# Kernel optimization log

Hardware: AMD Instinct MI355X
Metric: run time of the kernel (lower is better)

Reference implementation:

```python
import jax, jax.numpy as jnp
import numpy as np

B, HH, WW, C = 8, 56, 56, 192
DEPTH = 2
D_IN = 384      # ssm_ratio=2.0 * d_model
R = 12          # dt_rank = ceil(192/16)
HID = 768
L = HH * WW
EPS = 1e-5

PNAMES = ("norm1_w", "norm1_b", "in_proj_w", "conv_w", "conv_b", "x_proj_w",
          "dt_proj_w", "dt_proj_b", "A_log", "Ds", "out_norm_w", "out_norm_b",
          "out_proj_w", "norm2_w", "norm2_b", "fc1_w", "fc1_b", "fc2_w", "fc2_b")


def _mst_bfs_np(fm):
    """Per-image MST (Kruskal) on the 4-connected grid with cosine-distance
    edge weights mapped through exp (MinimumSpanningTree('Cosine', torch.exp)),
    then BFS from node 0. Returns (bfs order, parent-of-ordered-node)."""
    fm = np.asarray(fm, np.float32)
    Bn, H, W, Cc = fm.shape
    Ln = H * W
    idx_out = np.zeros((Bn, Ln), np.int32)
    par_out = np.zeros((Bn, Ln), np.int32)
    ids = np.arange(Ln).reshape(H, W)
    e_u = np.concatenate([ids[:, :-1].ravel(), ids[:-1, :].ravel()])
    e_v = np.concatenate([ids[:, 1:].ravel(), ids[1:, :].ravel()])
    for b in range(Bn):
        f = fm[b].reshape(Ln, Cc)
        nrm = np.linalg.norm(f, axis=1) + 1e-8
        cos = (f[e_u] * f[e_v]).sum(1) / (nrm[e_u] * nrm[e_v])
        wgt = np.exp(1.0 - cos)
        order = np.argsort(wgt, kind="stable")
        uf = np.arange(Ln)
        def find(a):
            while uf[a] != a:
                uf[a] = uf[uf[a]]
                a = uf[a]
            return a
        adj = [[] for _ in range(Ln)]
        cnt = 0
        for e in order:
            u, v = int(e_u[e]), int(e_v[e])
            ru, rv = find(u), find(v)
            if ru != rv:
                uf[ru] = rv
                adj[u].append(v)
                adj[v].append(u)
                cnt += 1
                if cnt == Ln - 1:
                    break
        bfs = np.zeros(Ln, np.int32)
        par = np.zeros(Ln, np.int32)
        visited = np.zeros(Ln, bool)
        visited[0] = True
        head, tail = 0, 1
        while head < tail:
            u = int(bfs[head])
            for v in adj[u]:
                if not visited[v]:
                    visited[v] = True
                    bfs[tail] = v
                    par[tail] = u
                    tail += 1
            head += 1
        idx_out[b] = bfs
        par_out[b] = par
    return idx_out, par_out


def _mst_bfs(x):
    shp = jax.ShapeDtypeStruct((x.shape[0], x.shape[1] * x.shape[2]), jnp.int32)
    return jax.pure_callback(_mst_bfs_np, (shp, shp), jax.lax.stop_gradient(x))


def _ln(x, w, b):
    mu = jnp.mean(x, -1, keepdims=True)
    var = jnp.mean((x - mu) ** 2, -1, keepdims=True)
    return (x - mu) * jax.lax.rsqrt(var + EPS) * w + b


def _tree_scan(feat, w, bfs_idx, bfs_par):
    # feat, w: (B, L, D); bfs_idx/bfs_par: (B, L) int32.
    # Pass 1 (leaf->root): S[p] += w[n] * S[n] in reverse BFS order.
    # Pass 2 (root->leaf): H[n] = S[n] + w[n] * (H[p] - w[n] * S[n]).
    Bn = feat.shape[0]
    bi = jnp.arange(Bn)

    def p1(S, np_):
        n, p = np_
        S = S.at[bi, p].add(w[bi, n] * S[bi, n])
        return S, None

    xs1 = (bfs_idx[:, 1:][:, ::-1].T, bfs_par[:, 1:][:, ::-1].T)
    S, _ = jax.lax.scan(p1, feat, xs1)

    def p2(Hc, np_):
        n, p = np_
        wn, sn = w[bi, n], S[bi, n]
        Hc = Hc.at[bi, n].set(sn + wn * (Hc[bi, p] - wn * sn))
        return Hc, None

    xs2 = (bfs_idx[:, 1:].T, bfs_par[:, 1:].T)
    Hh, _ = jax.lax.scan(p2, S, xs2)
    return Hh


def _layer(x, p, tree):
    bfs_idx, bfs_par = tree
    Bn = x.shape[0]
    # --- Tree_SSM branch (pre-norm) ---
    xn = _ln(x, p["norm1_w"], p["norm1_b"])
    xz = xn @ p["in_proj_w"].T                     # (B,H,W,2*D_IN)
    xs, z = jnp.split(xz, 2, axis=-1)
    xs = jax.lax.conv_general_dilated(
        xs, p["conv_w"], (1, 1), "SAME",
        dimension_numbers=("NHWC", "HWIO", "NHWC"),
        feature_group_count=D_IN) + p["conv_b"]    # depthwise 3x3
    u = jax.nn.silu(xs).reshape(Bn, L, D_IN)       # (B,L,D)
    x_dbl = u @ p["x_proj_w"].T                    # (B,L,R+2), d_state=1
    dts = jax.nn.softplus(x_dbl[..., :R] @ p["dt_proj_w"].T + p["dt_proj_b"])
    Bs, Cs = x_dbl[..., R:R + 1], x_dbl[..., R + 1:R + 2]
    A = -jnp.exp(p["A_log"][:, 0])                 # (D,)
    w = jnp.exp(dts * A)                           # edge decay to parent
    feat = dts * Bs * u                            # delta * B * u
    Hh = _tree_scan(feat, w, bfs_idx, bfs_par)
    y = (Cs * Hh + p["Ds"] * u).reshape(Bn, HH, WW, D_IN)
    y = _ln(y, p["out_norm_w"], p["out_norm_b"]) * jax.nn.silu(z)
    x = x + y @ p["out_proj_w"].T
    # --- MLP branch ---
    h = _ln(x, p["norm2_w"], p["norm2_b"])
    h = jax.nn.gelu(h @ p["fc1_w"].T + p["fc1_b"], approximate=False)
    return x + h @ p["fc2_w"].T + p["fc2_b"]


def setup_inputs() -> dict:
    key = jax.random.key(0)
    ks = jax.random.split(key, 12)
    n = jax.random.normal
    return {
        "x": n(ks[0], (B, HH, WW, C), jnp.float32),
        "norm1_w": jnp.ones((DEPTH, C)), "norm1_b": jnp.zeros((DEPTH, C)),
        "in_proj_w": n(ks[1], (DEPTH, 2 * D_IN, C)) * 0.02,
        "conv_w": n(ks[2], (DEPTH, 3, 3, 1, D_IN)) * 0.05,
        "conv_b": jnp.zeros((DEPTH, D_IN)),
        "x_proj_w": n(ks[3], (DEPTH, R + 2, D_IN)) * 0.02,
        "dt_proj_w": n(ks[4], (DEPTH, D_IN, R)) * 0.05,
        "dt_proj_b": n(ks[5], (DEPTH, D_IN)) * 0.1,
        "A_log": jnp.log(0.5 + jax.random.uniform(ks[6], (DEPTH, D_IN, 1))),
        "Ds": jax.random.uniform(ks[7], (DEPTH, D_IN)),
        "out_norm_w": jnp.ones((DEPTH, D_IN)), "out_norm_b": jnp.zeros((DEPTH, D_IN)),
        "out_proj_w": n(ks[8], (DEPTH, C, D_IN)) * 0.02,
        "norm2_w": jnp.ones((DEPTH, C)), "norm2_b": jnp.zeros((DEPTH, C)),
        "fc1_w": n(ks[9], (DEPTH, HID, C)) * 0.02, "fc1_b": jnp.zeros((DEPTH, HID)),
        "fc2_w": n(ks[10], (DEPTH, C, HID)) * 0.02, "fc2_b": jnp.zeros((DEPTH, C)),
        "fnorm_w": jnp.ones((C,)), "fnorm_b": jnp.zeros((C,)),
    }


def reference(x, norm1_w, norm1_b, in_proj_w, conv_w, conv_b, x_proj_w,
              dt_proj_w, dt_proj_b, A_log, Ds, out_norm_w, out_norm_b,
              out_proj_w, norm2_w, norm2_b, fc1_w, fc1_b, fc2_w, fc2_b,
              fnorm_w, fnorm_b):
    pvals = (norm1_w, norm1_b, in_proj_w, conv_w, conv_b, x_proj_w, dt_proj_w,
             dt_proj_b, A_log, Ds, out_norm_w, out_norm_b, out_proj_w, norm2_w,
             norm2_b, fc1_w, fc1_b, fc2_w, fc2_b)
    for i in range(DEPTH):
        pl = {k: v[i] for k, v in zip(PNAMES, pvals)}
        tree = _mst_bfs(x)  # input-adaptive MST, recomputed per layer
        x = _layer(x, pl, tree)
    return _ln(x, fnorm_w, fnorm_b)
```

## Files before the change

### kernel.cpp

```cpp
#include <hip/hip_runtime.h>
#include <math.h>

#define NB 8
#define NC 192
#define DIN 384
#define NL 3136
#define ROWS (NB*NL)
#define NE 6160
#define NHID 768

typedef unsigned short u16;
typedef unsigned int u32;
typedef unsigned long long u64;
typedef __attribute__((ext_vector_type(8))) short bh8;
typedef __attribute__((ext_vector_type(4))) float f4;

typedef __attribute__((address_space(1))) const void gl_as1;
typedef __attribute__((address_space(3))) void gl_as3;
#define GL16(g, l) __builtin_amdgcn_global_load_lds((gl_as1*)(const void*)(g), (gl_as3*)(void*)(l), 16, 0, 0)

__device__ __forceinline__ float wredsum(float v){
  v += __shfl_xor(v, 1, 64); v += __shfl_xor(v, 2, 64); v += __shfl_xor(v, 4, 64);
  v += __shfl_xor(v, 8, 64); v += __shfl_xor(v, 16, 64); v += __shfl_xor(v, 32, 64);
  return v;
}
__device__ __forceinline__ void edge_decode(int e, int& u, int& v){
  if (e < 3080){ int h = e/55, w = e - h*55; u = h*56 + w; v = u + 1; }
  else { int e2 = e - 3080; int h = e2/56, w = e2 - h*56; u = h*56 + w; v = u + 56; }
}
__device__ __forceinline__ float siluf(float x){ return x / (1.0f + expf(-x)); }
__device__ __forceinline__ float sofplus(float x){ return fmaxf(x, 0.0f) + log1pf(expf(-fabsf(x))); }
__device__ __forceinline__ float geluf(float x){ return 0.5f * x * (1.0f + erff(x * 0.70710678118654752f)); }
__device__ __forceinline__ u16 f2bf(float x){
  u32 u = __float_as_uint(x);
  u32 r = (u + 0x7fffu + ((u >> 16) & 1u)) >> 16;
  return (u16)r;
}
__device__ __forceinline__ float bf2f(u16 h){ return __uint_as_float(((u32)h) << 16); }

__global__ __launch_bounds__(256) void norms_kernel(const float* __restrict__ x, float* __restrict__ nrm){
  int gw = (int)((blockIdx.x * 256u + threadIdx.x) >> 6);
  int lane = threadIdx.x & 63;
  if (gw >= ROWS) return;
  const float* r = x + (size_t)gw * NC;
  float s = 0.f;
#pragma unroll
  for (int j = 0; j < 3; ++j){ float v = r[lane + 64*j]; s += v*v; }
  s = wredsum(s);
  if (lane == 0) nrm[gw] = sqrtf(s) + 1e-8f;
}

__global__ __launch_bounds__(256) void keys_kernel(const float* __restrict__ x, const float* __restrict__ nrm,
                                                   u64* __restrict__ keys){
  int gw = (int)((blockIdx.x * 256u + threadIdx.x) >> 6);
  int lane = threadIdx.x & 63;
  if (gw >= NB * NE) return;
  int b = gw / NE, e = gw - b * NE;
  int u, v; edge_decode(e, u, v);
  const float* ru = x + ((size_t)b * NL + u) * NC;
  const float* rv = x + ((size_t)b * NL + v) * NC;
  float s = 0.f;
#pragma unroll
  for (int j = 0; j < 3; ++j){ s += ru[lane + 64*j] * rv[lane + 64*j]; }
  s = wredsum(s);
  if (lane == 0){
    float cosv = s / (nrm[b*NL + u] * nrm[b*NL + v]);
    float wgt = expf(1.0f - cosv);
    keys[(size_t)b*NE + e] = ((u64)__float_as_uint(wgt) << 32) | (u64)(u32)e;
  }
}

__global__ __launch_bounds__(1024) void tree_kernel(const u64* __restrict__ keys_g,
      int* __restrict__ order_g, int* __restrict__ parpos_g, int* __restrict__ pos_g,
      int* __restrict__ lvl_g, int* __restrict__ nlev_g){
  __shared__ __align__(16) char sm[62736];
  const int b = blockIdx.x;
  const int t = threadIdx.x;
  const int NT = 1024;
  u64* best   = (u64*)sm;
  u16* parent = (u16*)(sm + 25088);
  u16* comp   = (u16*)(sm + 31360);
  u16* mstU   = (u16*)(sm + 37632);
  u16* mstV   = (u16*)(sm + 43904);
  u32* cnts   = (u32*)(sm + 56448);
  u16* adjl4  = (u16*)sm;
  u32* deg    = (u32*)(sm + 25088);
  u32* fr     = (u32*)(sm + 37632);
  u16* ppos   = (u16*)(sm + 50176);

  const u64* kb = keys_g + (size_t)b * NE;
  for (int v = t; v < NL; v += NT) parent[v] = (u16)v;
  if (t == 0){ cnts[0] = 0; cnts[3] = 0xffffffffu; }
  __syncthreads();

  u32 gpass = 0;
  for (int round = 0; round < 24; ++round){
    for (int it = 0; it < 12; ++it){
      int vv[4]; u16 pv[4]; int nb2 = 0;
#pragma unroll
      for (int j = 0; j < 4; ++j){ int v = t + j*NT; if (v < NL){ vv[nb2] = v; pv[nb2] = parent[v]; ++nb2; } }
      u16 gp[4];
      for (int j = 0; j < nb2; ++j) gp[j] = parent[pv[j]];
      bool ch = false;
      for (int j = 0; j < nb2; ++j){ if (gp[j] != pv[j]){ parent[vv[j]] = gp[j]; ch = true; } }
      bool docheck = (it & 1);
      if (docheck && ch) cnts[3] = gpass;
      __syncthreads();
      if (docheck){
        u32 seen = cnts[3];
        __syncthreads();
        u32 cur = gpass; ++gpass;
        if (seen != cur) break;
      }
    }
    for (int v = t; v < NL; v += NT){ comp[v] = parent[v]; best[v] = ~0ull; }
    if (t == 0) cnts[2] = 0;
    __syncthreads();
    {
      int ee[7]; int eu[7], ev[7]; u16 cu[7], cv[7]; u64 kk[7]; int nb2 = 0;
#pragma unroll
      for (int j = 0; j < 7; ++j){
        int e = t + j*NT;
        if (e < NE){ ee[nb2] = e; int u, v; edge_decode(e, u, v); eu[nb2] = u; ev[nb2] = v; ++nb2; }
      }
      for (int j = 0; j < nb2; ++j){ cu[j] = comp[eu[j]]; cv[j] = comp[ev[j]]; }
      for (int j = 0; j < nb2; ++j){ kk[j] = kb[ee[j]]; }
      for (int j = 0; j < nb2; ++j){
        if (cu[j] != cv[j]){
          atomicMin(&best[cu[j]], kk[j]);
          atomicMin(&best[cv[j]], kk[j]);
        }
      }
    }
    __syncthreads();
    {
      int rr[4]; u64 bk[4]; int nb2 = 0;
#pragma unroll
      for (int j = 0; j < 4; ++j){ int r = t + j*NT; if (r < NL){ rr[nb2] = r; ++nb2; } }
      u16 cr[4];
      for (int j = 0; j < nb2; ++j) cr[j] = comp[rr[j]];
      for (int j = 0; j < nb2; ++j) bk[j] = (cr[j] == (u16)rr[j]) ? best[rr[j]] : ~0ull;
      int uu[4], vv2[4]; u16 ru2[4], rv2[4];
      for (int j = 0; j < nb2; ++j){
        if (bk[j] != ~0ull){ int e = (int)(u32)bk[j]; edge_decode(e, uu[j], vv2[j]); }
      }
      for (int j = 0; j < nb2; ++j){
        if (bk[j] != ~0ull){ ru2[j] = comp[uu[j]]; rv2[j] = comp[vv2[j]]; }
      }
      for (int j = 0; j < nb2; ++j){
        if (bk[j] != ~0ull){
          int r = rr[j];
          u16 other = (ru2[j] == (u16)r) ? rv2[j] : ru2[j];
          bool mutual = (best[other] == bk[j]);
          if (!mutual || (u16)r < other){
            parent[r] = other;
            u32 id = atomicAdd(&cnts[0], 1);
            mstU[id] = (u16)uu[j]; mstV[id] = (u16)vv2[j];
            cnts[2] = 1;
          }
        }
      }
    }
    __syncthreads();
    if (cnts[0] >= (u32)(NL - 1) || cnts[2] == 0) break;
  }
  __syncthreads();

  const int nm = NL - 1;
  for (int v = t; v < NL; v += NT){
    deg[v] = 0;
    *(u64*)&adjl4[v*4] = 0xffffffffffffffffull;
  }
  __syncthreads();
  {
    int uu[4], vv2[4]; int nb2 = 0;
#pragma unroll
    for (int j = 0; j < 4; ++j){
      int i = t + j*NT;
      if (i < nm){ uu[nb2] = mstU[i]; vv2[nb2] = mstV[i]; ++nb2; }
    }
    for (int j = 0; j < nb2; ++j){
      u32 s1 = atomicAdd(&deg[uu[j]], 1); adjl4[uu[j]*4 + s1] = (u16)vv2[j];
      u32 s2 = atomicAdd(&deg[vv2[j]], 1); adjl4[vv2[j]*4 + s2] = (u16)uu[j];
    }
  }
  __syncthreads();

  if (t == 0){
    fr[0] = 0u | (0xffffu << 16);
    ppos[0] = 0;
    cnts[1] = 1;
    lvl_g[b*3200 + 0] = 0; lvl_g[b*3200 + 1] = 1;
  }
  __syncthreads();
  if (t < 64){
    int flo = 0, fhi = 1, d = 1;
    while (fhi < NL){
      for (int base2 = flo; base2 < fhi; base2 += 64){
        int idx = base2 + t;
        if (idx < fhi){
          u32 f = fr[idx];
          int u = (int)(f & 0xffffu), pn = (int)(f >> 16);
          u64 four = *(const u64*)&adjl4[u*4];
#pragma unroll
          for (int j = 0; j < 4; ++j){
            int v = (int)((four >> (16*j)) & 0xffffu);
            if (v != 0xffff && v != pn){
              u32 pos = atomicAdd(&cnts[1], 1);
              fr[pos] = (u32)v | ((u32)u << 16);
              ppos[pos] = (u16)idx;
            }
          }
        }
        asm volatile("s_waitcnt lgkmcnt(0)" ::: "memory");
      }
      int nf = (int)cnts[1];
      if (t == 0) lvl_g[b*3200 + d + 1] = nf;
      flo = fhi; fhi = nf; ++d;
      if (nf == flo) break;
    }
    if (t == 0) nlev_g[b] = d;
  }
  __syncthreads();

  for (int p = t; p < NL; p += NT){
    u32 f = fr[p];
    int node = (int)(f & 0xffffu);
    order_g[b*NL + p] = node;
    parpos_g[b*NL + p] = (int)ppos[p];
    pos_g[b*NL + node] = p;
  }
}

__global__ __launch_bounds__(64) void sched_kernel(const int* __restrict__ lvl_g, const int* __restrict__ nlev_g,
    u32* __restrict__ wsched_g, int* __restrict__ nwin_g){
  __shared__ int lvls[3200];
  int b = blockIdx.x;
  int lane = threadIdx.x;
  int d = nlev_g[b];
  for (int i = lane; i <= d; i += 64) lvls[i] = lvl_g[b*3200 + i];
  __syncthreads();
  u32* su = wsched_g + (size_t)b*6528;
  u32* sd = su + 3264;
  int nk = d - 1;
  for (int pass = 0; pass < 2; ++pass){
    u32* out = pass ? sd : su;
    int carry = 0;
    for (int c0 = 0; c0 < nk; c0 += 64){
      int kk = c0 + lane;
      bool valid = kk < nk;
      int lo = 0, hi = 0, wc = 0;
      if (valid){
        int dd = pass ? (1 + kk) : (d - 1 - kk);
        lo = lvls[dd]; hi = lvls[dd+1];
        wc = (hi - lo + 63) >> 6;
      }
      int inc = wc;
      for (int off = 1; off < 64; off <<= 1){
        int v = __shfl_up(inc, off, 64);
        if (lane >= off) inc += v;
      }
      int excl = carry + inc - wc;
      if (valid){
        for (int w = 0; w < wc; ++w){
          int base2 = lo + (w << 6);
          u32 e = (u32)base2 | ((u32)hi << 16);
          if (base2 + 64 >= hi) e |= 0x80000000u;
          out[excl + w] = e;
        }
      }
      carry += __shfl(inc, 63, 64);
    }
    if (lane == 0) nwin_g[b*2 + pass] = carry;
  }
}

template<int D, bool BF16OUT>
__global__ __launch_bounds__(256) void ln_kernel(const float* __restrict__ in, const float* __restrict__ g,
                                                 const float* __restrict__ bt, void* __restrict__ outv){
  int gw = (int)((blockIdx.x * 256u + threadIdx.x) >> 6);
  int lane = threadIdx.x & 63;
  if (gw >= ROWS) return;
  constexpr int J = D / 64;
  const float* r = in + (size_t)gw * D;
  float v[J]; float s = 0.f;
#pragma unroll
  for (int j = 0; j < J; ++j){ v[j] = r[lane + 64*j]; s += v[j]; }
  s = wredsum(s);
  float mu = s * (1.0f / D);
  float q = 0.f;
#pragma unroll
  for (int j = 0; j < J; ++j){ float dd = v[j] - mu; q += dd*dd; }
  q = wredsum(q);
  float rs = rsqrtf(q * (1.0f / D) + 1e-5f);
  if (BF16OUT){
    u16* o = (u16*)outv + (size_t)gw * D;
#pragma unroll
    for (int j = 0; j < J; ++j){
      int dch = lane + 64*j;
      float y = (v[j] - mu) * rs * g[dch] + bt[dch];
      o[dch] = f2bf(y);
    }
  } else {
    float* o = (float*)outv + (size_t)gw * D;
#pragma unroll
    for (int j = 0; j < J; ++j){ int dch = lane + 64*j; o[dch] = (v[j] - mu) * rs * g[dch] + bt[dch]; }
  }
}

__global__ __launch_bounds__(256) void wsplit_kernel(const float* __restrict__ W, u16* __restrict__ o, int N, int K){
  int i = blockIdx.x * 256 + threadIdx.x;
  if (i >= N * K) return;
  int r = i / K, c = i - r * K;
  float v = W[i];
  u16 hi = f2bf(v);
  o[(size_t)r * 2 * K + c] = hi;
  o[(size_t)r * 2 * K + K + c] = f2bf(v - bf2f(hi));
}

template<int BN, bool BIAS, int ACT, bool RESID, bool OBF16, bool DUALOUT>
__global__ __launch_bounds__(256) void mgemm_kernel(
    const u16* __restrict__ Ap, const u16* __restrict__ Wp,
    const float* __restrict__ bias, const float* __restrict__ resid,
    float* __restrict__ Cm, float* __restrict__ C2, int M, int N, int K){
  static_assert(BN == 64 || BN == 128, "BN");
  constexpr int WT = (BN == 128) ? 64 : 32;
  constexpr int NF = WT / 16;
  __shared__ short Ah[128*64];
  __shared__ short Wh[BN*64], Wl[BN*64];
  const int bm = blockIdx.y * 128, bn = blockIdx.x * BN;
  const int tid = threadIdx.x, lane = tid & 63, wid = tid >> 6;
  const int wr = wid >> 1, wc = wid & 1;
  const int K2 = 2 * K;
  f4 acc[4][NF];
#pragma unroll
  for (int mf = 0; mf < 4; ++mf)
#pragma unroll
    for (int nf = 0; nf < NF; ++nf) acc[mf][nf] = (f4){0.f,0.f,0.f,0.f};

  for (int k0 = 0; k0 < K; k0 += 64){
#pragma unroll
    for (int j = 0; j < 4; ++j){
      int isb = wid*4 + j;
      int r = isb*8 + (lane >> 3);
      int c = lane & 7;
      const u16* src = Ap + (size_t)(bm + r) * K + k0 + ((c ^ (r & 7)) << 3);
      GL16(src, &Ah[isb*512]);
    }
#pragma unroll
    for (int j = 0; j < BN/32; ++j){
      int isb = wid*(BN/32) + j;
      int r = isb*8 + (lane >> 3);
      int c = lane & 7;
      const u16* src = Wp + (size_t)(bn + r) * K2 + k0 + ((c ^ (r & 7)) << 3);
      GL16(src,     &Wh[isb*512]);
      GL16(src + K, &Wl[isb*512]);
    }
    __syncthreads();
#pragma unroll
    for (int kk = 0; kk < 2; ++kk){
      bh8 whf[NF], wlf[NF], ahf[4];
#pragma unroll
      for (int nf = 0; nf < NF; ++nf){
        int rw = wc*WT + nf*16 + (lane & 15);
        int c = kk*4 + (lane >> 4);
        int ad = rw*64 + ((c ^ (rw & 7)) * 8);
        whf[nf] = *(const bh8*)&Wh[ad];
        wlf[nf] = *(const bh8*)&Wl[ad];
      }
#pragma unroll
      for (int mf = 0; mf < 4; ++mf){
        int ra = wr*64 + mf*16 + (lane & 15);
        int c = kk*4 + (lane >> 4);
        int ad = ra*64 + ((c ^ (ra & 7)) * 8);
        ahf[mf] = *(const bh8*)&Ah[ad];
      }
#pragma unroll
      for (int mf = 0; mf < 4; ++mf)
#pragma unroll
        for (int nf = 0; nf < NF; ++nf){
          acc[mf][nf] = __builtin_amdgcn_mfma_f32_16x16x32_bf16(ahf[mf], whf[nf], acc[mf][nf], 0, 0, 0);
          acc[mf][nf] = __builtin_amdgcn_mfma_f32_16x16x32_bf16(ahf[mf], wlf[nf], acc[mf][nf], 0, 0, 0);
        }
    }
    __syncthreads();
  }
  const int cb = bn + wc*WT;
#pragma unroll
  for (int mf = 0; mf < 4; ++mf){
    int row = bm + wr*64 + mf*16 + (lane >> 4)*4;
#pragma unroll
    for (int nf = 0; nf < NF; ++nf){
      int col = cb + nf*16 + (lane & 15);
#pragma unroll
      for (int r = 0; r < 4; ++r){
        float v = acc[mf][nf][r];
        if (BIAS) v += bias[col];
        if (ACT == 1) v = geluf(v);
        if (RESID) v += resid[(size_t)(row + r) * N + col];
        if (DUALOUT){
          float* op = (col < 384) ? Cm : C2;
          int oc = (col < 384) ? col : col - 384;
          op[(size_t)(row + r) * 384 + oc] = v;
        } else if (OBF16){
          u16* op = (u16*)Cm;
          op[(size_t)(row + r) * N + col] = f2bf(v);
        } else {
          Cm[(size_t)(row + r) * N + col] = v;
        }
      }
    }
  }
}

__global__ __launch_bounds__(256) void conv_kernel(const float* __restrict__ xs, const float* __restrict__ cw,
                                                   const float* __restrict__ cb, float* __restrict__ u){
  int idx = blockIdx.x * 256 + threadIdx.x;
  if (idx >= ROWS * 96) return;
  int q = idx % 96; int l = idx / 96;
  int b = l / NL; int hw = l - b * NL; int h = hw / 56; int wc = hw - h * 56;
  int c4 = q * 4;
  float4 acc = *(const float4*)(cb + c4);
#pragma unroll
  for (int kh = 0; kh < 3; ++kh){
    int hh = h + kh - 1; if (hh < 0 || hh >= 56) continue;
#pragma unroll
    for (int kw = 0; kw < 3; ++kw){
      int wwc = wc + kw - 1; if (wwc < 0 || wwc >= 56) continue;
      float4 iv = *(const float4*)(xs + ((size_t)(b * NL + hh*56 + wwc)) * DIN + c4);
      float4 wv = *(const float4*)(cw + (size_t)(kh*3 + kw) * DIN + c4);
      acc.x += iv.x * wv.x; acc.y += iv.y * wv.y; acc.z += iv.z * wv.z; acc.w += iv.w * wv.w;
    }
  }
  float4 o; o.x = siluf(acc.x); o.y = siluf(acc.y); o.z = siluf(acc.z); o.w = siluf(acc.w);
  *(float4*)(u + (size_t)l * DIN + c4) = o;
}

__global__ __launch_bounds__(256) void xdbl_kernel(const float* __restrict__ u,
    const float* __restrict__ xpw, const float* __restrict__ dtw_g,
    const float* __restrict__ dtb, const float* __restrict__ alog, const int* __restrict__ pos_g,
    float* __restrict__ wout, float* __restrict__ fout, float* __restrict__ csout){
  __shared__ float xw[14*384];
  __shared__ float dw[384*12];
  __shared__ float db[384];
  __shared__ float An[384];
  int t = threadIdx.x;
  for (int i = t; i < 14*384; i += 256) xw[i] = xpw[i];
  for (int i = t; i < 384*12; i += 256) dw[i] = dtw_g[i];
  for (int i = t; i < 384; i += 256){ db[i] = dtb[i]; An[i] = -expf(alog[i]); }
  __syncthreads();
  int wave = t >> 6, lane = t & 63;
  int row0 = blockIdx.x * 16 + wave * 4;
  for (int rr = 0; rr < 4; ++rr){
    int m = row0 + rr;
    int b = m / NL;
    int pos = pos_g[m];
    size_t orow = ((size_t)b * NL + pos) * DIN;
    const float* ur = u + (size_t)m * DIN;
    float u6[6];
#pragma unroll
    for (int j = 0; j < 6; ++j) u6[j] = ur[lane + 64*j];
    float xd[14];
#pragma unroll
    for (int r = 0; r < 14; ++r){
      float p = 0.f;
#pragma unroll
      for (int j = 0; j < 6; ++j) p += u6[j] * xw[r*384 + lane + 64*j];
      xd[r] = wredsum(p);
    }
    float Bs = xd[12], Cv = xd[13];
#pragma unroll
    for (int j = 0; j < 6; ++j){
      int dch = lane + 64*j;
      float pre = db[dch];
#pragma unroll
      for (int r = 0; r < 12; ++r) pre += xd[r] * dw[dch*12 + r];
      float dts = sofplus(pre);
      float wv = expf(dts * An[dch]);
      float fv = dts * Bs * u6[j];
      wout[orow + dch] = wv;
      fout[orow + dch] = fv;
    }
    if (lane == 0) csout[m] = Cv;
  }
}

__global__ __launch_bounds__(256) void wtr_kernel(const float* __restrict__ in, float* __restrict__ out){
  __shared__ float tile[64][65];
  int blk = blockIdx.x;
  int b = blk / (49*6);
  int r = blk - b*(49*6);
  int pt = r / 6, ct = r - pt*6;
  int t = threadIdx.x;
  int tr = t >> 6, lane = t & 63;
  const float* src = in + ((size_t)b*NL + (size_t)pt*64) * DIN + ct*64;
#pragma unroll
  for (int k = 0; k < 16; ++k){
    int rr = tr + k*4;
    tile[rr][lane] = src[(size_t)rr*DIN + lane];
  }
  __syncthreads();
  float* dst = out + ((size_t)b*DIN + (size_t)ct*64) * NL + (size_t)pt*64;
#pragma unroll
  for (int k = 0; k < 16; ++k){
    int cc = tr + k*4;
    dst[(size_t)cc*NL + lane] = tile[lane][cc];
  }
}

template<bool UP>
__device__ __forceinline__ void sweep_run(const u32* __restrict__ sc, int nw,
    float* __restrict__ Sp, const float* __restrict__ wbase, const int* __restrict__ pg, int lane){
  if (nw <= 0) return;
  u32 d0 = sc[lane];
  u32 d1 = sc[64 + lane];
  int curch = 0;
  float wA = 0.f, wB = 0.f; int pA = 0, pB = 0;
  int baseA = 0, hiA = 0, baseB = 0, hiB = 0;
  u32 eA = 0, eB = 0; bool aA = false, aB = false;
  {
    u32 dc = __shfl(d0, 0, 64);
    baseA = (int)(dc & 0xffffu); hiA = (int)((dc >> 16) & 0x7fffu); eA = dc >> 31;
    int p = baseA + lane; aA = p < hiA;
    if (aA){ wA = wbase[p]; pA = pg[p]; }
  }
  if (nw > 1){
    u32 dc = __shfl(d0, 1, 64);
    baseB = (int)(dc & 0xffffu); hiB = (int)((dc >> 16) & 0x7fffu); eB = dc >> 31;
    int p = baseB + lane; aB = p < hiB;
    if (aB){ wB = wbase[p]; pB = pg[p]; }
  }
  for (int iw = 0; iw < nw; ++iw){
    int ch = iw >> 6;
    if (ch != curch){ d0 = d1; d1 = sc[(ch + 1)*64 + lane]; curch = ch; }
    float wN = 0.f; int pN = 0; int baseN = 0, hiN = 0; u32 eN = 0; bool aN = false;
    int iw2 = iw + 2;
    if (iw2 < nw){
      int ch2 = iw2 >> 6;
      u32 dc2 = __shfl((ch2 == curch) ? d0 : d1, iw2 & 63, 64);
      baseN = (int)(dc2 & 0xffffu); hiN = (int)((dc2 >> 16) & 0x7fffu); eN = dc2 >> 31;
      int p = baseN + lane; aN = p < hiN;
      if (aN){ wN = wbase[p]; pN = pg[p]; }
    }
    int p = baseA + lane;
    if (aA){
      if (UP){
        float s = Sp[p];
        atomicAdd(&Sp[pA], wA * s);
      } else {
        float s = Sp[p]; float h = Sp[pA];
        Sp[p] = s + wA * (h - wA * s);
      }
    }
    if (eA){
      asm volatile("s_waitcnt lgkmcnt(0)" ::: "memory");
    }
    baseA = baseB; hiA = hiB; aA = aB; wA = wB; pA = pB; eA = eB;
    baseB = baseN; hiB = hiN; aB = aN; wB = wN; pB = pN; eB = eN;
  }
}

__global__ __launch_bounds__(256) void sweep8_kernel(const float* __restrict__ featp, const float* __restrict__ wtr,
    float* __restrict__ Hp, const int* __restrict__ parpos_g,
    const u32* __restrict__ wsched_g, const int* __restrict__ nwin_g){
  __shared__ float S[4*NL];
  int blk = blockIdx.x;
  int b = blk & 7, q = blk >> 3;
  int t = threadIdx.x, lane = t & 63, wv = t >> 6;
  const int* pg = parpos_g + b*NL;
  const float* fbase = featp + (size_t)b*NL*DIN + q*4;
  const float* wbase = wtr + ((size_t)b*DIN + q*4 + wv) * NL;
  float*       hbase = Hp    + (size_t)b*NL*DIN + q*4;
  for (int i = t; i < NL; i += 256){
    float4 f = *(const float4*)(fbase + (size_t)i*DIN);
    S[0*NL + i] = f.x; S[1*NL + i] = f.y; S[2*NL + i] = f.z; S[3*NL + i] = f.w;
  }
  __syncthreads();
  float* Sp = &S[wv*NL];

  const u32* su = wsched_g + (size_t)b*6528;
  const u32* sd = su + 3264;
  int nwu = nwin_g[b*2], nwd = nwin_g[b*2 + 1];
  sweep_run<true>(su, nwu, Sp, wbase, pg, lane);
  sweep_run<false>(sd, nwd, Sp, wbase, pg, lane);

  __syncthreads();
  for (int i = t; i < NL; i += 256){
    float4 o;
    o.x = S[0*NL + i]; o.y = S[1*NL + i]; o.z = S[2*NL + i]; o.w = S[3*NL + i];
    *(float4*)(hbase + (size_t)i*DIN) = o;
  }
}

__global__ __launch_bounds__(256) void ynorm_kernel(const float* __restrict__ Hp, const float* __restrict__ u,
    const float* __restrict__ z, const float* __restrict__ Cs, const int* __restrict__ order_g,
    const float* __restrict__ Ds, const float* __restrict__ g, const float* __restrict__ bt,
    u16* __restrict__ out){
  int gw = (int)((blockIdx.x * 256u + threadIdx.x) >> 6);
  int lane = threadIdx.x & 63;
  if (gw >= ROWS) return;
  int b = gw / NL;
  int node = order_g[gw];
  size_t nrow = (size_t)b * NL + node;
  float Cv = Cs[nrow];
  const float* hr = Hp + (size_t)gw * DIN;
  const float* ur = u + nrow * DIN;
  const float* zr = z + nrow * DIN;
  float y[6]; float s = 0.f;
#pragma unroll
  for (int j = 0; j < 6; ++j){
    int dch = lane + 64*j;
    y[j] = Cv * hr[dch] + Ds[dch] * ur[dch];
    s += y[j];
  }
  s = wredsum(s);
  float mu = s * (1.0f / DIN);
  float q = 0.f;
#pragma unroll
  for (int j = 0; j < 6; ++j){ float dd = y[j] - mu; q += dd*dd; }
  q = wredsum(q);
  float rs = rsqrtf(q * (1.0f / DIN) + 1e-5f);
  u16* o = out + nrow * DIN;
#pragma unroll
  for (int j = 0; j < 6; ++j){
    int dch = lane + 64*j;
    float yn = (y[j] - mu) * rs * g[dch] + bt[dch];
    float v = yn * siluf(zr[dch]);
    o[dch] = f2bf(v);
  }
}

extern "C" void kernel_launch(void* const* d_in, const int* in_sizes, int n_in,
                              void* d_out, int out_size, void* d_ws, size_t ws_size,
                              hipStream_t stream){
  const float* x_in       = (const float*)d_in[0];
  const float* norm1_w    = (const float*)d_in[1];
  const float* norm1_b    = (const float*)d_in[2];
  const float* in_proj_w  = (const float*)d_in[3];
  const float* conv_w     = (const float*)d_in[4];
  const float* conv_b     = (const float*)d_in[5];
  const float* x_proj_w   = (const float*)d_in[6];
  const float* dt_proj_w  = (const float*)d_in[7];
  const float* dt_proj_b  = (const float*)d_in[8];
  const float* A_log      = (const float*)d_in[9];
  const float* Ds         = (const float*)d_in[10];
  const float* out_norm_w = (const float*)d_in[11];
  const float* out_norm_b = (const float*)d_in[12];
  const float* out_proj_w = (const float*)d_in[13];
  const float* norm2_w    = (const float*)d_in[14];
  const float* norm2_b    = (const float*)d_in[15];
  const float* fc1_w      = (const float*)d_in[16];
  const float* fc1_b      = (const float*)d_in[17];
  const float* fc2_w      = (const float*)d_in[18];
  const float* fc2_b      = (const float*)d_in[19];
  const float* fnorm_w    = (const float*)d_in[20];
  const float* fnorm_b    = (const float*)d_in[21];

  float* ws = (float*)d_ws;
  float* X     = ws + 0;
  u16*   bufAh = (u16*)(ws + 4816896);
  float* bufZ  = ws + 9633792;
  float* bufW  = ws + 19267584;
  float* bufU  = ws + 28901376;
  float* bufF  = ws + 38535168;
  u16*   Gp    = (u16*)bufU;
  float* Csb   = ws + 48168960;
  int*   ordg  = (int*)(ws + 48194048);
  int*   ppg   = (int*)(ws + 48219136);
  int*   lvlg  = (int*)(ws + 48244224);
  int*   nlvg  = (int*)(ws + 48269824);
  u64*   keysg = (u64*)(ws + 48269832);
  float* nrm   = ws + 48368392;
  u16*   ipWp  = (u16*)(ws + 48393480);
  u16*   opWp  = (u16*)(ws + 48540936);
  u16*   fc1Wp = (u16*)(ws + 48614664);
  u16*   fc2Wp = (u16*)(ws + 48762120);
  int*   posg  = (int*)(ws + 48909576);
  float* wtrp  = ws + 48934664;
  u32*   wschg = (u32*)(ws + 58568456);
  int*   nwing = (int*)(ws + 58620680);

  hipMemcpyAsync(X, x_in, (size_t)ROWS * NC * sizeof(float), hipMemcpyDeviceToDevice, stream);

  for (int i = 0; i < 2; ++i){
    wsplit_kernel<<<(768*192+255)/256, 256, 0, stream>>>(in_proj_w + (size_t)i*NHID*NC, ipWp, 768, 192);
    wsplit_kernel<<<(192*384+255)/256, 256, 0, stream>>>(out_proj_w + (size_t)i*NC*DIN, opWp, 192, 384);
    wsplit_kernel<<<(768*192+255)/256, 256, 0, stream>>>(fc1_w + (size_t)i*NHID*NC, fc1Wp, 768, 192);
    wsplit_kernel<<<(192*768+255)/256, 256, 0, stream>>>(fc2_w + (size_t)i*NC*NHID, fc2Wp, 192, 768);

    norms_kernel<<<ROWS/4, 256, 0, stream>>>(X, nrm);
    keys_kernel<<<(NB*NE)/4, 256, 0, stream>>>(X, nrm, keysg);
    tree_kernel<<<NB, 1024, 0, stream>>>(keysg, ordg, ppg, posg, lvlg, nlvg);
    sched_kernel<<<NB, 64, 0, stream>>>(lvlg, nlvg, wschg, nwing);

    ln_kernel<192,true><<<ROWS/4, 256, 0, stream>>>(X, norm1_w + i*NC, norm1_b + i*NC, bufAh);
    mgemm_kernel<128,false,0,false,false,true><<<dim3(6,196), 256, 0, stream>>>(bufAh, ipWp, nullptr, nullptr, bufF, bufZ, ROWS, 768, 192);

    conv_kernel<<<(ROWS*96)/256, 256, 0, stream>>>(bufF, conv_w + (size_t)i*9*DIN, conv_b + i*DIN, bufU);

    xdbl_kernel<<<ROWS/16, 256, 0, stream>>>(bufU, x_proj_w + (size_t)i*14*DIN, dt_proj_w + (size_t)i*DIN*12,
                                             dt_proj_b + i*DIN, A_log + i*DIN, posg, bufW, bufF, Csb);

    wtr_kernel<<<8*49*6, 256, 0, stream>>>(bufW, wtrp);

    sweep8_kernel<<<NB*96, 256, 0, stream>>>(bufF, wtrp, bufF, ppg, wschg, nwing);

    ynorm_kernel<<<ROWS/4, 256, 0, stream>>>(bufF, bufU, bufZ, Csb, ordg, Ds + i*DIN,
                                             out_norm_w + i*DIN, out_norm_b + i*DIN, (u16*)bufW);

    mgemm_kernel<64,false,0,true,false,false><<<dim3(3,196), 256, 0, stream>>>((u16*)bufW, opWp, nullptr, X, X, nullptr, ROWS, 192, 384);

    ln_kernel<192,true><<<ROWS/4, 256, 0, stream>>>(X, norm2_w + i*NC, norm2_b + i*NC, bufAh);
    mgemm_kernel<128,true,1,false,true,false><<<dim3(6,196), 256, 0, stream>>>(bufAh, fc1Wp, fc1_b + i*NHID, nullptr, (float*)Gp, nullptr, ROWS, NHID, 192);
    mgemm_kernel<64,true,0,true,false,false><<<dim3(3,196), 256, 0, stream>>>(Gp, fc2Wp, fc2_b + i*NC, X, X, nullptr, ROWS, 192, 768);
  }

  ln_kernel<192,false><<<ROWS/4, 256, 0, stream>>>(X, fnorm_w, fnorm_b, d_out);
}
```

Measured before the change: 1.514 ms.

## Fuse MST tree build with in-projection GEMM in one heterogeneous launch

Merges the serial per-image tree kernel (8 blocks) with the in-projection GEMM into a single launch. The first 8 blocks build the trees and the rest do the GEMM tiles, so the latency-bound tree work overlaps with GEMM work instead of leaving most CUs idle. The tree kernel is rewritten for 256 threads instead of 1024, with chunked loops. This cuts its per-block parallelism, so the critical tree path may get longer, and the GEMM blocks must share 62KB LDS sizing.

```diff
diff --git a/kernel.cpp b/kernel.cpp
--- a/kernel.cpp
+++ b/kernel.cpp
@@ -70,13 +70,11 @@
   }
 }
 
-__global__ __launch_bounds__(1024) void tree_kernel(const u64* __restrict__ keys_g,
+__device__ void tree_body(char* sm, int b, const u64* __restrict__ keys_g,
       int* __restrict__ order_g, int* __restrict__ parpos_g, int* __restrict__ pos_g,
       int* __restrict__ lvl_g, int* __restrict__ nlev_g){
-  __shared__ __align__(16) char sm[62736];
-  const int b = blockIdx.x;
   const int t = threadIdx.x;
-  const int NT = 1024;
+  const int NT = 256;
   u64* best   = (u64*)sm;
   u16* parent = (u16*)(sm + 25088);
   u16* comp   = (u16*)(sm + 31360);
@@ -96,13 +94,15 @@
   u32 gpass = 0;
   for (int round = 0; round < 24; ++round){
     for (int it = 0; it < 12; ++it){
-      int vv[4]; u16 pv[4]; int nb2 = 0;
-#pragma unroll
-      for (int j = 0; j < 4; ++j){ int v = t + j*NT; if (v < NL){ vv[nb2] = v; pv[nb2] = parent[v]; ++nb2; } }
-      u16 gp[4];
-      for (int j = 0; j < nb2; ++j) gp[j] = parent[pv[j]];
       bool ch = false;
-      for (int j = 0; j < nb2; ++j){ if (gp[j] != pv[j]){ parent[vv[j]] = gp[j]; ch = true; } }
+      for (int c0 = 0; c0 < NL; c0 += NT*4){
+        int vv[4]; u16 pv[4]; int nb2 = 0;
+#pragma unroll
+        for (int j = 0; j < 4; ++j){ int v = c0 + t + j*NT; if (v < NL){ vv[nb2] = v; pv[nb2] = parent[v]; ++nb2; } }
+        u16 gp[4];
+        for (int j = 0; j < nb2; ++j) gp[j] = parent[pv[j]];
+        for (int j = 0; j < nb2; ++j){ if (gp[j] != pv[j]){ parent[vv[j]] = gp[j]; ch = true; } }
+      }
       bool docheck = (it & 1);
       if (docheck && ch) cnts[3] = gpass;
       __syncthreads();
@@ -116,11 +116,11 @@
     for (int v = t; v < NL; v += NT){ comp[v] = parent[v]; best[v] = ~0ull; }
     if (t == 0) cnts[2] = 0;
     __syncthreads();
-    {
-      int ee[7]; int eu[7], ev[7]; u16 cu[7], cv[7]; u64 kk[7]; int nb2 = 0;
-#pragma unroll
-      for (int j = 0; j < 7; ++j){
-        int e = t + j*NT;
+    for (int c0 = 0; c0 < NE; c0 += NT*8){
+      int ee[8]; int eu[8], ev[8]; u16 cu[8], cv[8]; u64 kk[8]; int nb2 = 0;
+#pragma unroll
+      for (int j = 0; j < 8; ++j){
+        int e = c0 + t + j*NT;
         if (e < NE){ ee[nb2] = e; int u, v; edge_decode(e, u, v); eu[nb2] = u; ev[nb2] = v; ++nb2; }
       }
       for (int j = 0; j < nb2; ++j){ cu[j] = comp[eu[j]]; cv[j] = comp[ev[j]]; }
@@ -133,10 +133,10 @@
       }
     }
     __syncthreads();
-    {
+    for (int c0 = 0; c0 < NL; c0 += NT*4){
       int rr[4]; u64 bk[4]; int nb2 = 0;
 #pragma unroll
-      for (int j = 0; j < 4; ++j){ int r = t + j*NT; if (r < NL){ rr[nb2] = r; ++nb2; } }
+      for (int j = 0; j < 4; ++j){ int r = c0 + t + j*NT; if (r < NL){ rr[nb2] = r; ++nb2; } }
       u16 cr[4];
       for (int j = 0; j < nb2; ++j) cr[j] = comp[rr[j]];
       for (int j = 0; j < nb2; ++j) bk[j] = (cr[j] == (u16)rr[j]) ? best[rr[j]] : ~0ull;
@@ -172,11 +172,11 @@
     *(u64*)&adjl4[v*4] = 0xffffffffffffffffull;
   }
   __syncthreads();
-  {
+  for (int c0 = 0; c0 < nm; c0 += NT*4){
     int uu[4], vv2[4]; int nb2 = 0;
 #pragma unroll
     for (int j = 0; j < 4; ++j){
-      int i = t + j*NT;
+      int i = c0 + t + j*NT;
       if (i < nm){ uu[nb2] = mstU[i]; vv2[nb2] = mstV[i]; ++nb2; }
     }
     for (int j = 0; j < nb2; ++j){
@@ -229,6 +229,100 @@
     order_g[b*NL + p] = node;
     parpos_g[b*NL + p] = (int)ppos[p];
     pos_g[b*NL + node] = p;
+  }
+}
+
+__device__ void inproj_body(char* sm, int bid, const u16* __restrict__ Ap, const u16* __restrict__ Wp,
+                            float* __restrict__ Cm, float* __restrict__ C2){
+  const int K = 192, K2 = 384;
+  short* Ah = (short*)sm;
+  short* Wh = (short*)(sm + 16384);
+  short* Wl = (short*)(sm + 32768);
+  const int bn = (bid % 6) * 128, bm = (bid / 6) * 128;
+  const int tid = threadIdx.x, lane = tid & 63, wid = tid >> 6;
+  const int wr = wid >> 1, wc = wid & 1;
+  f4 acc[4][4];
+#pragma unroll
+  for (int mf = 0; mf < 4; ++mf)
+#pragma unroll
+    for (int nf = 0; nf < 4; ++nf) acc[mf][nf] = (f4){0.f,0.f,0.f,0.f};
+
+  for (int k0 = 0; k0 < K; k0 += 64){
+#pragma unroll
+    for (int j = 0; j < 4; ++j){
+      int isb = wid*4 + j;
+      int r = isb*8 + (lane >> 3);
+      int c = lane & 7;
+      const u16* src = Ap + (size_t)(bm + r) * K + k0 + ((c ^ (r & 7)) << 3);
+      GL16(src, &Ah[isb*512]);
+    }
+#pragma unroll
+    for (int j = 0; j < 4; ++j){
+      int isb = wid*4 + j;
+      int r = isb*8 + (lane >> 3);
+      int c = lane & 7;
+      const u16* src = Wp + (size_t)(bn + r) * K2 + k0 + ((c ^ (r & 7)) << 3);
+      GL16(src,     &Wh[isb*512]);
+      GL16(src + K, &Wl[isb*512]);
+    }
+    __syncthreads();
+#pragma unroll
+    for (int kk = 0; kk < 2; ++kk){
+      bh8 whf[4], wlf[4], ahf[4];
+#pragma unroll
+      for (int nf = 0; nf < 4; ++nf){
+        int rw = wc*64 + nf*16 + (lane & 15);
+        int c = kk*4 + (lane >> 4);
+        int ad = rw*64 + ((c ^ (rw & 7)) * 8);
+        whf[nf] = *(const bh8*)&Wh[ad];
+        wlf[nf] = *(const bh8*)&Wl[ad];
+      }
+#pragma unroll
+      for (int mf = 0; mf < 4; ++mf){
+        int ra = wr*64 + mf*16 + (lane & 15);
+        int c = kk*4 + (lane >> 4);
+        int ad = ra*64 + ((c ^ (ra & 7)) * 8);
+        ahf[mf] = *(const bh8*)&Ah[ad];
+      }
+#pragma unroll
+      for (int mf = 0; mf < 4; ++mf)
+#pragma unroll
+        for (int nf = 0; nf < 4; ++nf){
+          acc[mf][nf] = __builtin_amdgcn_mfma_f32_16x16x32_bf16(ahf[mf], whf[nf], acc[mf][nf], 0, 0, 0);
+          acc[mf][nf] = __builtin_amdgcn_mfma_f32_16x16x32_bf16(ahf[mf], wlf[nf], acc[mf][nf], 0, 0, 0);
+        }
+    }
+    __syncthreads();
+  }
+  const int cb = bn + wc*64;
+#pragma unroll
+  for (int mf = 0; mf < 4; ++mf){
+    int row = bm + wr*64 + mf*16 + (lane >> 4)*4;
+#pragma unroll
+    for (int nf = 0; nf < 4; ++nf){
+      int col = cb + nf*16 + (lane & 15);
+#pragma unroll
+      for (int r = 0; r < 4; ++r){
+        float v = acc[mf][nf][r];
+        float* op = (col < 384) ? Cm : C2;
+        int oc = (col < 384) ? col : col - 384;
+        op[(size_t)(row + r) * 384 + oc] = v;
+      }
+    }
+  }
+}
+
+__global__ __launch_bounds__(256) void fused_tree_inproj(
+    const u64* __restrict__ keysg, int* __restrict__ ordg, int* __restrict__ ppg,
+    int* __restrict__ posg, int* __restrict__ lvlg, int* __restrict__ nlvg,
+    const u16* __restrict__ Ap, const u16* __restrict__ Wp,
+    float* __restrict__ Cm, float* __restrict__ C2){
+  __shared__ __align__(16) char sm[62736];
+  int bid = blockIdx.x;
+  if (bid < 8){
+    tree_body(sm, bid, keysg, ordg, ppg, posg, lvlg, nlvg);
+  } else {
+    inproj_body(sm, bid - 8, Ap, Wp, Cm, C2);
   }
 }
 
@@ -690,11 +784,13 @@
 
     norms_kernel<<<ROWS/4, 256, 0, stream>>>(X, nrm);
     keys_kernel<<<(NB*NE)/4, 256, 0, stream>>>(X, nrm, keysg);
-    tree_kernel<<<NB, 1024, 0, stream>>>(keysg, ordg, ppg, posg, lvlg, nlvg);
+
+    ln_kernel<192,true><<<ROWS/4, 256, 0, stream>>>(X, norm1_w + i*NC, norm1_b + i*NC, bufAh);
+
+    fused_tree_inproj<<<8 + 6*196, 256, 0, stream>>>(keysg, ordg, ppg, posg, lvlg, nlvg,
+                                                     bufAh, ipWp, bufF, bufZ);
+
     sched_kernel<<<NB, 64, 0, stream>>>(lvlg, nlvg, wschg, nwing);
-
-    ln_kernel<192,true><<<ROWS/4, 256, 0, stream>>>(X, norm1_w + i*NC, norm1_b + i*NC, bufAh);
-    mgemm_kernel<128,false,0,false,false,true><<<dim3(6,196), 256, 0, stream>>>(bufAh, ipWp, nullptr, nullptr, bufF, bufZ, ROWS, 768, 192);
 
     conv_kernel<<<(ROWS*96)/256, 256, 0, stream>>>(bufF, conv_w + (size_t)i*9*DIN, conv_b + i*DIN, bufU);
 
```

Result: faster. 1.459 ms (-3.6%).
